# Performance work log

Hardware: AMD Instinct MI355X
Metric: run time of the kernel (lower is better)

The kernel has to match this reference:

```python
import jax, jax.numpy as jnp
import numpy as np

NUM_HEADS = 16
ROPE_BASE = 10000.0

def _rope(x):
    # x: (B, T, H, hd), rotate-half 1D RoPE over temporal axis
    B, T, H, hd = x.shape
    inv_freq = 1.0 / (ROPE_BASE ** (jnp.arange(0, hd, 2, dtype=jnp.float32) / hd))  # (hd/2,)
    freqs = jnp.arange(T, dtype=jnp.float32)[:, None] * inv_freq[None, :]            # (T, hd/2)
    emb = jnp.concatenate([freqs, freqs], axis=-1)                                    # (T, hd)
    cos = jnp.cos(emb)[None, :, None, :]
    sin = jnp.sin(emb)[None, :, None, :]
    x1, x2 = jnp.split(x, 2, axis=-1)
    rot = jnp.concatenate([-x2, x1], axis=-1)
    return x * cos + rot * sin

def setup_inputs() -> dict:
    key = jax.random.key(0)
    ks = jax.random.split(key, 7)
    B, T, S, D = 4, 16, 256, 2048
    std = 0.02
    return {
        'v_p': jax.random.normal(ks[0], (B, T, S, D), jnp.float32),
        'v_f': jax.random.normal(ks[1], (B, T, S, D), jnp.float32),
        'a_p': jax.random.normal(ks[2], (B, T, D), jnp.float32),
        'a_f': jax.random.normal(ks[3], (B, T, D), jnp.float32),
        'W_qkv': jax.random.normal(ks[4], (D, 3 * D), jnp.float32) * std,
        'W_proj': jax.random.normal(ks[5], (D, D), jnp.float32) * std,
        'b_proj': jnp.zeros((D,), jnp.float32),
    }

def reference(v_p, v_f, a_p, a_f, W_qkv, W_proj, b_proj):
    B, T_p, S, D = v_p.shape
    T_f = v_f.shape[1]
    H = NUM_HEADS
    hd = D // H
    scale = hd ** -0.5
    # pool spatial dim and concatenate streams: [v_p, v_f, a_p, a_f]
    tokens = jnp.concatenate([v_p.mean(axis=2), v_f.mean(axis=2), a_p, a_f], axis=1)  # (B, T, D)
    T = tokens.shape[1]
    qkv = tokens @ W_qkv  # qkv_bias=False
    q, k, v = jnp.split(qkv, 3, axis=-1)
    q = q.reshape(B, T, H, hd)
    k = k.reshape(B, T, H, hd)
    v = v.reshape(B, T, H, hd)
    q = _rope(q)
    k = _rope(k)
    scores = jnp.einsum('bqhd,bkhd->bhqk', q, k) * scale
    causal_mask = jnp.triu(jnp.ones((T, T), dtype=bool), k=1)
    scores = jnp.where(causal_mask[None, None], -jnp.inf, scores)
    attn = jax.nn.softmax(scores, axis=-1)
    out = jnp.einsum('bhqk,bkhd->bqhd', attn, v).reshape(B, T, D)
    out = out @ W_proj + b_proj
    v_p_out = jnp.broadcast_to(out[:, :T_p, None, :], (B, T_p, S, D))
    v_f_out = jnp.broadcast_to(out[:, T_p:T_p + T_f, None, :], (B, T_f, S, D))
    a_p_out = out[:, T_p + T_f:T_p + T_f + T_p]
    a_f_out = out[:, T_p + T_f + T_p:]
    return (v_p_out, v_f_out, a_p_out, a_f_out)
```

## Files before the change

kernel.cpp:

```cpp
#include <hip/hip_runtime.h>
#include <hip/hip_bf16.h>
#include <stdint.h>


using bf16x8v = __attribute__((ext_vector_type(8))) __bf16;
using f32x4v  = __attribute__((ext_vector_type(4))) float;

union Pack8 { __bf16 h[8]; uint4 u; };
union Pack4 { __bf16 h[4]; uint2 u; };

__device__ __forceinline__ int swz(int r, int c) {
    return (r << 6) + ((c ^ (r & 7)) << 3);
}
__device__ __forceinline__ int aswz(int r, int c) {
    return (r << 7) + ((c ^ (r & 31)) << 2);
}

__global__ __launch_bounds__(256) void prep_mean_kernel(
    const float* __restrict__ v_p, const float* __restrict__ v_f,
    float* __restrict__ partials,
    const float* __restrict__ W_qkv, const float* __restrict__ W_proj,
    __bf16* __restrict__ Wt_qkv, __bf16* __restrict__ Wt_proj)
{
    __shared__ float Ls[64][68];
    int bid0 = blockIdx.x;
    if (bid0 < 2048) {
        int bid = bid0;
        int which  = bid >> 10;
        int rem    = bid & 1023;
        int row    = rem >> 4;
        int dchunk = (rem >> 3) & 1;
        int schunk = rem & 7;
        int d = (dchunk << 10) + (threadIdx.x << 2);
        const float* src = (which ? v_f : v_p) + ((size_t)row << 19)
                         + ((size_t)(schunk << 5) << 11) + d;
        float4 a = {0.f, 0.f, 0.f, 0.f};
        #pragma unroll 8
        for (int s = 0; s < 32; ++s) {
            float4 x = *reinterpret_cast<const float4*>(src + ((size_t)s << 11));
            a.x += x.x; a.y += x.y; a.z += x.z; a.w += x.w;
        }
        int pr = which * 64 + row;
        *reinterpret_cast<float4*>(&partials[(size_t)((pr << 3) + schunk) * 2048 + d]) = a;
    } else {
        int bid = bid0 - 2048;
        const float* src; __bf16* dst; int N, tile;
        if (bid < 3072) { src = W_qkv;  dst = Wt_qkv;  N = 6144; tile = bid; }
        else            { src = W_proj; dst = Wt_proj; N = 2048; tile = bid - 3072; }
        int tiles_n = N >> 6;
        int tn = tile % tiles_n;
        int tk = tile / tiles_n;
        int t = threadIdx.x;
        int rb = t >> 4;
        int c4 = (t & 15) << 2;
        #pragma unroll
        for (int s = 0; s < 4; ++s) {
            int r = rb + (s << 4);
            float4 v = *reinterpret_cast<const float4*>(
                src + (size_t)(tk * 64 + r) * N + tn * 64 + c4);
            *reinterpret_cast<float4*>(&Ls[r][c4]) = v;
        }
        __syncthreads();
        int c  = t >> 2;
        int r0 = (t & 3) << 4;
        Pack8 p0, p1;
        #pragma unroll
        for (int i = 0; i < 8; ++i) p0.h[i] = (__bf16)Ls[r0 + i][c];
        #pragma unroll
        for (int i = 0; i < 8; ++i) p1.h[i] = (__bf16)Ls[r0 + 8 + i][c];
        __bf16* drow = dst + (size_t)(tn * 64 + c) * 2048 + tk * 64 + r0;
        *reinterpret_cast<uint4*>(drow)     = p0.u;
        *reinterpret_cast<uint4*>(drow + 8) = p1.u;
    }
}

__global__ __launch_bounds__(256) void tokens_finish_kernel(
    const float* __restrict__ partials, const float* __restrict__ a_p,
    const float* __restrict__ a_f, __bf16* __restrict__ tokens_bf)
{
    int bid = blockIdx.x;
    if (bid < 128) {
        int idx = (bid * 256 + threadIdx.x) * 8;
        int r = idx >> 11;
        int d = idx & 2047;
        float s[8];
        #pragma unroll
        for (int i = 0; i < 8; ++i) s[i] = 0.f;
        #pragma unroll
        for (int sc = 0; sc < 8; ++sc) {
            const float* p = partials + (size_t)((r << 3) + sc) * 2048 + d;
            float4 x0 = *reinterpret_cast<const float4*>(p);
            float4 x1 = *reinterpret_cast<const float4*>(p + 4);
            s[0] += x0.x; s[1] += x0.y; s[2] += x0.z; s[3] += x0.w;
            s[4] += x1.x; s[5] += x1.y; s[6] += x1.z; s[7] += x1.w;
        }
        const float inv = 1.f / 256.f;
        int which = r >> 6, rr = r & 63;
        int b = rr >> 4, tt = rr & 15;
        int tokrow = b * 64 + which * 16 + tt;
        Pack8 p;
        #pragma unroll
        for (int i = 0; i < 8; ++i) p.h[i] = (__bf16)(s[i] * inv);
        *reinterpret_cast<uint4*>(&tokens_bf[(size_t)tokrow * 2048 + d]) = p.u;
    } else {
        int g = (bid - 128) * 256 + threadIdx.x;
        int which = g >> 14;
        int j = g & 16383;
        int b = j >> 12;
        int rr = j & 4095;
        int tt = rr >> 8;
        int gq = rr & 255;
        const float* src = (which ? a_f : a_p) + (size_t)(b * 16 + tt) * 2048 + gq * 8;
        float4 x0 = *reinterpret_cast<const float4*>(src);
        float4 x1 = *reinterpret_cast<const float4*>(src + 4);
        Pack8 p;
        p.h[0] = (__bf16)x0.x; p.h[1] = (__bf16)x0.y; p.h[2] = (__bf16)x0.z; p.h[3] = (__bf16)x0.w;
        p.h[4] = (__bf16)x1.x; p.h[5] = (__bf16)x1.y; p.h[6] = (__bf16)x1.z; p.h[7] = (__bf16)x1.w;
        int tokrow = b * 64 + 32 + which * 16 + tt;
        *reinterpret_cast<uint4*>(&tokens_bf[(size_t)tokrow * 2048 + gq * 8]) = p.u;
    }
}

__global__ __launch_bounds__(256) void gemm_bf16_kernel(
    const __bf16* __restrict__ A, const __bf16* __restrict__ Bt,
    const float* __restrict__ bias, float* __restrict__ C, int N)
{
    __shared__ __bf16 As[4096];
    __shared__ __bf16 Bs[4096];
    const int t = threadIdx.x;
    const int m0 = blockIdx.y << 6;
    const int n0 = blockIdx.x << 6;
    const int lane = t & 63;
    const int w = t >> 6;
    const int wm = w << 4;
    const int lrow = lane & 15;
    const int lk = lane >> 4;
    const int srl = lane >> 3;
    const int schunk = lane & 7;

    f32x4v acc[4] = {{0.f,0.f,0.f,0.f},{0.f,0.f,0.f,0.f},
                     {0.f,0.f,0.f,0.f},{0.f,0.f,0.f,0.f}};

    int row_c0 = (w << 4) + srl;
    int row_c1 = row_c0 + 8;
    const __bf16* gA0 = A  + (size_t)(m0 + row_c0) * 2048 + ((schunk ^ (row_c0 & 7)) << 3);
    const __bf16* gA1 = A  + (size_t)(m0 + row_c1) * 2048 + ((schunk ^ (row_c1 & 7)) << 3);
    const __bf16* gB0 = Bt + (size_t)(n0 + row_c0) * 2048 + ((schunk ^ (row_c0 & 7)) << 3);
    const __bf16* gB1 = Bt + (size_t)(n0 + row_c1) * 2048 + ((schunk ^ (row_c1 & 7)) << 3);
    __bf16* lA0 = &As[(w << 4) << 6];
    __bf16* lA1 = &As[((w << 4) + 8) << 6];
    __bf16* lB0 = &Bs[(w << 4) << 6];
    __bf16* lB1 = &Bs[((w << 4) + 8) << 6];

    for (int kt = 0; kt < 32; ++kt) {
        __syncthreads();
        int ko = kt << 6;
        __builtin_amdgcn_global_load_lds(
            (const __attribute__((address_space(1))) void*)(gA0 + ko),
            (__attribute__((address_space(3))) void*)lA0, 16, 0, 0);
        __builtin_amdgcn_global_load_lds(
            (const __attribute__((address_space(1))) void*)(gA1 + ko),
            (__attribute__((address_space(3))) void*)lA1, 16, 0, 0);
        __builtin_amdgcn_global_load_lds(
            (const __attribute__((address_space(1))) void*)(gB0 + ko),
            (__attribute__((address_space(3))) void*)lB0, 16, 0, 0);
        __builtin_amdgcn_global_load_lds(
            (const __attribute__((address_space(1))) void*)(gB1 + ko),
            (__attribute__((address_space(3))) void*)lB1, 16, 0, 0);
        __syncthreads();
        #pragma unroll
        for (int s = 0; s < 2; ++s) {
            int cA = (s << 2) + lk;
            bf16x8v af = *reinterpret_cast<const bf16x8v*>(&As[swz(wm + lrow, cA)]);
            #pragma unroll
            for (int j = 0; j < 4; ++j) {
                bf16x8v bf = *reinterpret_cast<const bf16x8v*>(&Bs[swz((j << 4) + lrow, cA)]);
                acc[j] = __builtin_amdgcn_mfma_f32_16x16x32_bf16(af, bf, acc[j], 0, 0, 0);
            }
        }
    }
    #pragma unroll
    for (int j = 0; j < 4; ++j) {
        int col = n0 + (j << 4) + lrow;
        float bv = bias ? bias[col] : 0.f;
        #pragma unroll
        for (int e = 0; e < 4; ++e) {
            int row = m0 + wm + (lk << 2) + e;
            C[(size_t)row * N + col] = acc[j][e] + bv;
        }
    }
}

__global__ __launch_bounds__(256) void attn_kernel(
    const float* __restrict__ qkv, __bf16* __restrict__ attn_out)
{
    __shared__ float q_s[64 * 128];
    __shared__ float k_s[64 * 128];
    int b = blockIdx.x >> 4;
    int h = blockIdx.x & 15;
    int tid = threadIdx.x;
    const float* base = qkv + (size_t)(b * 64) * 6144 + h * 128;
    const float L2C = 0.20762050593046012f;
    #pragma unroll
    for (int r = 0; r < 4; ++r) {
        int idx = tid + (r << 8);
        int tq = idx >> 4;
        int cg = idx & 15;
        int d = cg << 2;
        const float* srcr = base + (size_t)tq * 6144;
        float4 q1 = *reinterpret_cast<const float4*>(srcr + d);
        float4 q2 = *reinterpret_cast<const float4*>(srcr + d + 64);
        float4 k1 = *reinterpret_cast<const float4*>(srcr + 2048 + d);
        float4 k2 = *reinterpret_cast<const float4*>(srcr + 2048 + d + 64);
        float ft = (float)tq;
        float a0 = ft * exp2f(-(float)(d + 0) * L2C);
        float a1 = ft * exp2f(-(float)(d + 1) * L2C);
        float a2 = ft * exp2f(-(float)(d + 2) * L2C);
        float a3 = ft * exp2f(-(float)(d + 3) * L2C);
        float c0 = cosf(a0), s0 = sinf(a0);
        float c1 = cosf(a1), s1 = sinf(a1);
        float c2 = cosf(a2), s2 = sinf(a2);
        float c3 = cosf(a3), s3 = sinf(a3);
        float4 qa, qb, ka, kb;
        qa.x = q1.x * c0 - q2.x * s0;  qb.x = q2.x * c0 + q1.x * s0;
        qa.y = q1.y * c1 - q2.y * s1;  qb.y = q2.y * c1 + q1.y * s1;
        qa.z = q1.z * c2 - q2.z * s2;  qb.z = q2.z * c2 + q1.z * s2;
        qa.w = q1.w * c3 - q2.w * s3;  qb.w = q2.w * c3 + q1.w * s3;
        ka.x = k1.x * c0 - k2.x * s0;  kb.x = k2.x * c0 + k1.x * s0;
        ka.y = k1.y * c1 - k2.y * s1;  kb.y = k2.y * c1 + k1.y * s1;
        ka.z = k1.z * c2 - k2.z * s2;  kb.z = k2.z * c2 + k1.z * s2;
        ka.w = k1.w * c3 - k2.w * s3;  kb.w = k2.w * c3 + k1.w * s3;
        *reinterpret_cast<float4*>(&q_s[aswz(tq, cg)])      = qa;
        *reinterpret_cast<float4*>(&q_s[aswz(tq, cg + 16)]) = qb;
        *reinterpret_cast<float4*>(&k_s[aswz(tq, cg)])      = ka;
        *reinterpret_cast<float4*>(&k_s[aswz(tq, cg + 16)]) = kb;
    }
    __syncthreads();
    int qi = tid >> 2;
    int g  = tid & 3;
    float pv[16];
    #pragma unroll
    for (int j = 0; j < 16; ++j) pv[j] = 0.f;
    for (int c = 0; c < 32; ++c) {
        float4 a = *reinterpret_cast<const float4*>(&q_s[aswz(qi, c)]);
        #pragma unroll
        for (int j = 0; j < 16; ++j) {
            int ki = (j << 2) + g;
            float4 bb = *reinterpret_cast<const float4*>(&k_s[aswz(ki, c)]);
            pv[j] += a.x * bb.x + a.y * bb.y + a.z * bb.z + a.w * bb.w;
        }
    }
    const float scale = 0.0883883476483184405f;
    float m = -1e30f;
    #pragma unroll
    for (int j = 0; j < 16; ++j) {
        int ki = (j << 2) + g;
        pv[j] = (ki <= qi) ? pv[j] * scale : -1e30f;
        m = fmaxf(m, pv[j]);
    }
    m = fmaxf(m, __shfl_xor(m, 1));
    m = fmaxf(m, __shfl_xor(m, 2));
    float l = 0.f;
    #pragma unroll
    for (int j = 0; j < 16; ++j) {
        float e = (pv[j] > -1e29f) ? expf(pv[j] - m) : 0.f;
        pv[j] = e;
        l += e;
    }
    l += __shfl_xor(l, 1);
    l += __shfl_xor(l, 2);
    float inv_l = 1.f / l;
    __syncthreads();
    float* p_s = q_s;
    #pragma unroll
    for (int j = 0; j < 16; ++j) p_s[qi * 65 + (j << 2) + g] = pv[j] * inv_l;
    float* v_s = k_s;
    #pragma unroll
    for (int r = 0; r < 8; ++r) {
        int idx = tid + (r << 8);
        int tv = idx >> 5;
        int c = idx & 31;
        *reinterpret_cast<float4*>(&v_s[aswz(tv, c)]) =
            *reinterpret_cast<const float4*>(base + (size_t)tv * 6144 + 4096 + (c << 2));
    }
    __syncthreads();
    float4 acc[8];
    #pragma unroll
    for (int u = 0; u < 8; ++u) acc[u] = {0.f, 0.f, 0.f, 0.f};
    for (int ki = 0; ki < 64; ++ki) {
        float p = p_s[qi * 65 + ki];
        #pragma unroll
        for (int u = 0; u < 8; ++u) {
            float4 vv = *reinterpret_cast<const float4*>(&v_s[aswz(ki, g + (u << 2))]);
            acc[u].x += p * vv.x;
            acc[u].y += p * vv.y;
            acc[u].z += p * vv.z;
            acc[u].w += p * vv.w;
        }
    }
    __bf16* orow = attn_out + (size_t)(b * 64 + qi) * 2048 + h * 128 + (g << 2);
    #pragma unroll
    for (int u = 0; u < 8; ++u) {
        Pack4 p4;
        p4.h[0] = (__bf16)acc[u].x; p4.h[1] = (__bf16)acc[u].y;
        p4.h[2] = (__bf16)acc[u].z; p4.h[3] = (__bf16)acc[u].w;
        *reinterpret_cast<uint2*>(orow + (u << 4)) = p4.u;
    }
}

__global__ __launch_bounds__(256) void outputs_kernel(
    const float* __restrict__ outp, float* __restrict__ d_out)
{
    int bid = blockIdx.x;
    if (bid < 2048) {
        int which = bid >> 10;
        int rem = bid & 1023;
        int row = rem >> 4;
        int schunk = rem & 15;
        int b = row >> 4;
        int t = row & 15;
        const float* src = outp + (size_t)(b * 64 + (which << 4) + t) * 2048 + threadIdx.x * 8;
        float4 o0 = *reinterpret_cast<const float4*>(src);
        float4 o1 = *reinterpret_cast<const float4*>(src + 4);
        size_t base = (size_t)which * 33554432 +
                      ((size_t)row * 256 + (size_t)schunk * 16) * 2048 + threadIdx.x * 8;
        float* dst = d_out + base;
        #pragma unroll
        for (int s = 0; s < 16; ++s) {
            *reinterpret_cast<float4*>(dst + (size_t)s * 2048)     = o0;
            *reinterpret_cast<float4*>(dst + (size_t)s * 2048 + 4) = o1;
        }
    } else {
        int g8 = (bid - 2048) * 256 + threadIdx.x;
        int which = g8 >> 14;
        int j = g8 & 16383;
        int b = j >> 12;
        int rr = j & 4095;
        int tt = rr >> 8;
        int gq = rr & 255;
        const float* src = outp + (size_t)(b * 64 + 32 + (which << 4) + tt) * 2048 + gq * 8;
        float4 x0 = *reinterpret_cast<const float4*>(src);
        float4 x1 = *reinterpret_cast<const float4*>(src + 4);
        float* dst = d_out + 67108864 + (size_t)which * 131072 +
                     (size_t)(b * 16 + tt) * 2048 + gq * 8;
        *reinterpret_cast<float4*>(dst)     = x0;
        *reinterpret_cast<float4*>(dst + 4) = x1;
    }
}

extern "C" void kernel_launch(void* const* d_in, const int* in_sizes, int n_in,
                              void* d_out, int out_size, void* d_ws, size_t ws_size,
                              hipStream_t stream)
{
    const float* v_p    = (const float*)d_in[0];
    const float* v_f    = (const float*)d_in[1];
    const float* a_p    = (const float*)d_in[2];
    const float* a_f    = (const float*)d_in[3];
    const float* W_qkv  = (const float*)d_in[4];
    const float* W_proj = (const float*)d_in[5];
    const float* b_proj = (const float*)d_in[6];
    float* out_f = (float*)d_out;

    char* ws = (char*)d_ws;
    __bf16* tokens_bf = (__bf16*)(ws);
    __bf16* Wt_qkv    = (__bf16*)(ws + 1048576);
    __bf16* Wt_proj   = (__bf16*)(ws + 26214400);
    float*  qkv       = (float*)(ws + 34603008);
    __bf16* attn_bf   = (__bf16*)(ws + 40894464);
    float*  outp      = (float*)(ws + 41943040);
    float*  partials  = (float*)(ws + 44040192);

    prep_mean_kernel<<<6144, 256, 0, stream>>>(v_p, v_f, partials,
                                               W_qkv, W_proj, Wt_qkv, Wt_proj);
    tokens_finish_kernel<<<256, 256, 0, stream>>>(partials, a_p, a_f, tokens_bf);
    gemm_bf16_kernel<<<dim3(96, 4), 256, 0, stream>>>(tokens_bf, Wt_qkv, nullptr, qkv, 6144);
    attn_kernel<<<64, 256, 0, stream>>>(qkv, attn_bf);
    gemm_bf16_kernel<<<dim3(32, 4), 256, 0, stream>>>(attn_bf, Wt_proj, b_proj, outp, 2048);
    outputs_kernel<<<2176, 256, 0, stream>>>(outp, out_f);
}
```

Baseline: 218.7 us.

## Split-K both GEMMs by two and reduce partials in consumer kernels

Both bf16 GEMMs now split the K dimension into two halves across blockIdx.z, writing two partial output buffers instead of one. The attention kernel sums the two QKV partials when loading q/k/v, and the outputs kernel sums the two projection partials and adds the bias. This doubles the number of blocks on small GEMM grids (384 and 128 blocks) to fill more CUs, at the cost of extra partial-buffer traffic and additional loads in the consumers.

```diff
diff --git a/kernel.cpp b/kernel.cpp
--- a/kernel.cpp
+++ b/kernel.cpp
@@ -123,13 +123,15 @@
 
 __global__ __launch_bounds__(256) void gemm_bf16_kernel(
     const __bf16* __restrict__ A, const __bf16* __restrict__ Bt,
-    const float* __restrict__ bias, float* __restrict__ C, int N)
+    float* __restrict__ C, int N)
 {
     __shared__ __bf16 As[4096];
     __shared__ __bf16 Bs[4096];
     const int t = threadIdx.x;
     const int m0 = blockIdx.y << 6;
     const int n0 = blockIdx.x << 6;
+    const int kz = blockIdx.z;
+    const int kbase = kz << 10;
     const int lane = t & 63;
     const int w = t >> 6;
     const int wm = w << 4;
@@ -143,16 +145,16 @@
 
     int row_c0 = (w << 4) + srl;
     int row_c1 = row_c0 + 8;
-    const __bf16* gA0 = A  + (size_t)(m0 + row_c0) * 2048 + ((schunk ^ (row_c0 & 7)) << 3);
-    const __bf16* gA1 = A  + (size_t)(m0 + row_c1) * 2048 + ((schunk ^ (row_c1 & 7)) << 3);
-    const __bf16* gB0 = Bt + (size_t)(n0 + row_c0) * 2048 + ((schunk ^ (row_c0 & 7)) << 3);
-    const __bf16* gB1 = Bt + (size_t)(n0 + row_c1) * 2048 + ((schunk ^ (row_c1 & 7)) << 3);
+    const __bf16* gA0 = A  + (size_t)(m0 + row_c0) * 2048 + kbase + ((schunk ^ (row_c0 & 7)) << 3);
+    const __bf16* gA1 = A  + (size_t)(m0 + row_c1) * 2048 + kbase + ((schunk ^ (row_c1 & 7)) << 3);
+    const __bf16* gB0 = Bt + (size_t)(n0 + row_c0) * 2048 + kbase + ((schunk ^ (row_c0 & 7)) << 3);
+    const __bf16* gB1 = Bt + (size_t)(n0 + row_c1) * 2048 + kbase + ((schunk ^ (row_c1 & 7)) << 3);
     __bf16* lA0 = &As[(w << 4) << 6];
     __bf16* lA1 = &As[((w << 4) + 8) << 6];
     __bf16* lB0 = &Bs[(w << 4) << 6];
     __bf16* lB1 = &Bs[((w << 4) + 8) << 6];
 
-    for (int kt = 0; kt < 32; ++kt) {
+    for (int kt = 0; kt < 16; ++kt) {
         __syncthreads();
         int ko = kt << 6;
         __builtin_amdgcn_global_load_lds(
@@ -179,14 +181,14 @@
             }
         }
     }
+    float* Cz = C + (size_t)kz * 256 * N;
     #pragma unroll
     for (int j = 0; j < 4; ++j) {
         int col = n0 + (j << 4) + lrow;
-        float bv = bias ? bias[col] : 0.f;
         #pragma unroll
         for (int e = 0; e < 4; ++e) {
             int row = m0 + wm + (lk << 2) + e;
-            C[(size_t)row * N + col] = acc[j][e] + bv;
+            Cz[(size_t)row * N + col] = acc[j][e];
         }
     }
 }
@@ -196,10 +198,12 @@
 {
     __shared__ float q_s[64 * 128];
     __shared__ float k_s[64 * 128];
+    const size_t PART = (size_t)256 * 6144;
     int b = blockIdx.x >> 4;
     int h = blockIdx.x & 15;
     int tid = threadIdx.x;
-    const float* base = qkv + (size_t)(b * 64) * 6144 + h * 128;
+    const float* base0 = qkv + (size_t)(b * 64) * 6144 + h * 128;
+    const float* base1 = base0 + PART;
     const float L2C = 0.20762050593046012f;
     #pragma unroll
     for (int r = 0; r < 4; ++r) {
@@ -207,29 +211,38 @@
         int tq = idx >> 4;
         int cg = idx & 15;
         int d = cg << 2;
-        const float* srcr = base + (size_t)tq * 6144;
-        float4 q1 = *reinterpret_cast<const float4*>(srcr + d);
-        float4 q2 = *reinterpret_cast<const float4*>(srcr + d + 64);
-        float4 k1 = *reinterpret_cast<const float4*>(srcr + 2048 + d);
-        float4 k2 = *reinterpret_cast<const float4*>(srcr + 2048 + d + 64);
+        const float* s0 = base0 + (size_t)tq * 6144;
+        const float* s1 = base1 + (size_t)tq * 6144;
+        float4 q1a = *reinterpret_cast<const float4*>(s0 + d);
+        float4 q1b = *reinterpret_cast<const float4*>(s1 + d);
+        float4 q2a = *reinterpret_cast<const float4*>(s0 + d + 64);
+        float4 q2b = *reinterpret_cast<const float4*>(s1 + d + 64);
+        float4 k1a = *reinterpret_cast<const float4*>(s0 + 2048 + d);
+        float4 k1b = *reinterpret_cast<const float4*>(s1 + 2048 + d);
+        float4 k2a = *reinterpret_cast<const float4*>(s0 + 2048 + d + 64);
+        float4 k2b = *reinterpret_cast<const float4*>(s1 + 2048 + d + 64);
+        float4 q1 = {q1a.x + q1b.x, q1a.y + q1b.y, q1a.z + q1b.z, q1a.w + q1b.w};
+        float4 q2 = {q2a.x + q2b.x, q2a.y + q2b.y, q2a.z + q2b.z, q2a.w + q2b.w};
+        float4 k1 = {k1a.x + k1b.x, k1a.y + k1b.y, k1a.z + k1b.z, k1a.w + k1b.w};
+        float4 k2 = {k2a.x + k2b.x, k2a.y + k2b.y, k2a.z + k2b.z, k2a.w + k2b.w};
         float ft = (float)tq;
         float a0 = ft * exp2f(-(float)(d + 0) * L2C);
         float a1 = ft * exp2f(-(float)(d + 1) * L2C);
         float a2 = ft * exp2f(-(float)(d + 2) * L2C);
         float a3 = ft * exp2f(-(float)(d + 3) * L2C);
-        float c0 = cosf(a0), s0 = sinf(a0);
-        float c1 = cosf(a1), s1 = sinf(a1);
-        float c2 = cosf(a2), s2 = sinf(a2);
-        float c3 = cosf(a3), s3 = sinf(a3);
+        float c0 = cosf(a0), s0f = sinf(a0);
+        float c1 = cosf(a1), s1f = sinf(a1);
+        float c2 = cosf(a2), s2f = sinf(a2);
+        float c3 = cosf(a3), s3f = sinf(a3);
         float4 qa, qb, ka, kb;
-        qa.x = q1.x * c0 - q2.x * s0;  qb.x = q2.x * c0 + q1.x * s0;
-        qa.y = q1.y * c1 - q2.y * s1;  qb.y = q2.y * c1 + q1.y * s1;
-        qa.z = q1.z * c2 - q2.z * s2;  qb.z = q2.z * c2 + q1.z * s2;
-        qa.w = q1.w * c3 - q2.w * s3;  qb.w = q2.w * c3 + q1.w * s3;
-        ka.x = k1.x * c0 - k2.x * s0;  kb.x = k2.x * c0 + k1.x * s0;
-        ka.y = k1.y * c1 - k2.y * s1;  kb.y = k2.y * c1 + k1.y * s1;
-        ka.z = k1.z * c2 - k2.z * s2;  kb.z = k2.z * c2 + k1.z * s2;
-        ka.w = k1.w * c3 - k2.w * s3;  kb.w = k2.w * c3 + k1.w * s3;
+        qa.x = q1.x * c0 - q2.x * s0f;  qb.x = q2.x * c0 + q1.x * s0f;
+        qa.y = q1.y * c1 - q2.y * s1f;  qb.y = q2.y * c1 + q1.y * s1f;
+        qa.z = q1.z * c2 - q2.z * s2f;  qb.z = q2.z * c2 + q1.z * s2f;
+        qa.w = q1.w * c3 - q2.w * s3f;  qb.w = q2.w * c3 + q1.w * s3f;
+        ka.x = k1.x * c0 - k2.x * s0f;  kb.x = k2.x * c0 + k1.x * s0f;
+        ka.y = k1.y * c1 - k2.y * s1f;  kb.y = k2.y * c1 + k1.y * s1f;
+        ka.z = k1.z * c2 - k2.z * s2f;  kb.z = k2.z * c2 + k1.z * s2f;
+        ka.w = k1.w * c3 - k2.w * s3f;  kb.w = k2.w * c3 + k1.w * s3f;
         *reinterpret_cast<float4*>(&q_s[aswz(tq, cg)])      = qa;
         *reinterpret_cast<float4*>(&q_s[aswz(tq, cg + 16)]) = qb;
         *reinterpret_cast<float4*>(&k_s[aswz(tq, cg)])      = ka;
@@ -280,8 +293,10 @@
         int idx = tid + (r << 8);
         int tv = idx >> 5;
         int c = idx & 31;
-        *reinterpret_cast<float4*>(&v_s[aswz(tv, c)]) =
-            *reinterpret_cast<const float4*>(base + (size_t)tv * 6144 + 4096 + (c << 2));
+        float4 va = *reinterpret_cast<const float4*>(base0 + (size_t)tv * 6144 + 4096 + (c << 2));
+        float4 vb = *reinterpret_cast<const float4*>(base1 + (size_t)tv * 6144 + 4096 + (c << 2));
+        float4 vs = {va.x + vb.x, va.y + vb.y, va.z + vb.z, va.w + vb.w};
+        *reinterpret_cast<float4*>(&v_s[aswz(tv, c)]) = vs;
     }
     __syncthreads();
     float4 acc[8];
@@ -309,8 +324,10 @@
 }
 
 __global__ __launch_bounds__(256) void outputs_kernel(
-    const float* __restrict__ outp, float* __restrict__ d_out)
-{
+    const float* __restrict__ outp, const float* __restrict__ b_proj,
+    float* __restrict__ d_out)
+{
+    const size_t PART = (size_t)256 * 2048;
     int bid = blockIdx.x;
     if (bid < 2048) {
         int which = bid >> 10;
@@ -319,9 +336,19 @@
         int schunk = rem & 15;
         int b = row >> 4;
         int t = row & 15;
-        const float* src = outp + (size_t)(b * 64 + (which << 4) + t) * 2048 + threadIdx.x * 8;
-        float4 o0 = *reinterpret_cast<const float4*>(src);
-        float4 o1 = *reinterpret_cast<const float4*>(src + 4);
+        size_t srcoff = (size_t)(b * 64 + (which << 4) + t) * 2048 + threadIdx.x * 8;
+        const float* s0 = outp + srcoff;
+        const float* s1 = outp + PART + srcoff;
+        float4 a0 = *reinterpret_cast<const float4*>(s0);
+        float4 a1 = *reinterpret_cast<const float4*>(s0 + 4);
+        float4 b0 = *reinterpret_cast<const float4*>(s1);
+        float4 b1 = *reinterpret_cast<const float4*>(s1 + 4);
+        float4 v0 = *reinterpret_cast<const float4*>(b_proj + threadIdx.x * 8);
+        float4 v1 = *reinterpret_cast<const float4*>(b_proj + threadIdx.x * 8 + 4);
+        float4 o0 = {a0.x + b0.x + v0.x, a0.y + b0.y + v0.y,
+                     a0.z + b0.z + v0.z, a0.w + b0.w + v0.w};
+        float4 o1 = {a1.x + b1.x + v1.x, a1.y + b1.y + v1.y,
+                     a1.z + b1.z + v1.z, a1.w + b1.w + v1.w};
         size_t base = (size_t)which * 33554432 +
                       ((size_t)row * 256 + (size_t)schunk * 16) * 2048 + threadIdx.x * 8;
         float* dst = d_out + base;
@@ -338,9 +365,19 @@
         int rr = j & 4095;
         int tt = rr >> 8;
         int gq = rr & 255;
-        const float* src = outp + (size_t)(b * 64 + 32 + (which << 4) + tt) * 2048 + gq * 8;
-        float4 x0 = *reinterpret_cast<const float4*>(src);
-        float4 x1 = *reinterpret_cast<const float4*>(src + 4);
+        size_t srcoff = (size_t)(b * 64 + 32 + (which << 4) + tt) * 2048 + gq * 8;
+        const float* s0 = outp + srcoff;
+        const float* s1 = outp + PART + srcoff;
+        float4 a0 = *reinterpret_cast<const float4*>(s0);
+        float4 a1 = *reinterpret_cast<const float4*>(s0 + 4);
+        float4 b0 = *reinterpret_cast<const float4*>(s1);
+        float4 b1 = *reinterpret_cast<const float4*>(s1 + 4);
+        float4 v0 = *reinterpret_cast<const float4*>(b_proj + gq * 8);
+        float4 v1 = *reinterpret_cast<const float4*>(b_proj + gq * 8 + 4);
+        float4 x0 = {a0.x + b0.x + v0.x, a0.y + b0.y + v0.y,
+                     a0.z + b0.z + v0.z, a0.w + b0.w + v0.w};
+        float4 x1 = {a1.x + b1.x + v1.x, a1.y + b1.y + v1.y,
+                     a1.z + b1.z + v1.z, a1.w + b1.w + v1.w};
         float* dst = d_out + 67108864 + (size_t)which * 131072 +
                      (size_t)(b * 16 + tt) * 2048 + gq * 8;
         *reinterpret_cast<float4*>(dst)     = x0;
@@ -366,15 +403,15 @@
     __bf16* Wt_qkv    = (__bf16*)(ws + 1048576);
     __bf16* Wt_proj   = (__bf16*)(ws + 26214400);
     float*  qkv       = (float*)(ws + 34603008);
-    __bf16* attn_bf   = (__bf16*)(ws + 40894464);
-    float*  outp      = (float*)(ws + 41943040);
-    float*  partials  = (float*)(ws + 44040192);
+    __bf16* attn_bf   = (__bf16*)(ws + 47185920);
+    float*  outp      = (float*)(ws + 48234496);
+    float*  partials  = (float*)(ws + 52428800);
 
     prep_mean_kernel<<<6144, 256, 0, stream>>>(v_p, v_f, partials,
                                                W_qkv, W_proj, Wt_qkv, Wt_proj);
     tokens_finish_kernel<<<256, 256, 0, stream>>>(partials, a_p, a_f, tokens_bf);
-    gemm_bf16_kernel<<<dim3(96, 4), 256, 0, stream>>>(tokens_bf, Wt_qkv, nullptr, qkv, 6144);
+    gemm_bf16_kernel<<<dim3(96, 4, 2), 256, 0, stream>>>(tokens_bf, Wt_qkv, qkv, 6144);
     attn_kernel<<<64, 256, 0, stream>>>(qkv, attn_bf);
-    gemm_bf16_kernel<<<dim3(32, 4), 256, 0, stream>>>(attn_bf, Wt_proj, b_proj, outp, 2048);
-    outputs_kernel<<<2176, 256, 0, stream>>>(outp, out_f);
-}
+    gemm_bf16_kernel<<<dim3(32, 4, 2), 256, 0, stream>>>(attn_bf, Wt_proj, outp, 2048);
+    outputs_kernel<<<2176, 256, 0, stream>>>(outp, b_proj, out_f);
+}
```

Measured after the change: 203.5 us. 6.9% less time.
